# Optimization experiments

Measured on AMD Instinct MI355X. Metric: run time of the kernel, lower is better.

## Reference

```python
import jax, jax.numpy as jnp
import numpy as np

B, S, H = 4, 2048, 1024
HEADS = 16
DFF = 4 * H
EPS = 1e-12


def _layer_norm(x, w, b):
    mu = jnp.mean(x, axis=-1, keepdims=True)
    var = jnp.mean(jnp.square(x - mu), axis=-1, keepdims=True)
    return (x - mu) * jax.lax.rsqrt(var + EPS) * w + b


def setup_inputs() -> dict:
    key = jax.random.key(0)
    ks = jax.random.split(key, 12)
    sc = 0.02
    return {
        "input": jax.random.normal(ks[0], (B, S, H), dtype=jnp.float32),
        "input_mask": jnp.zeros((B, 1, 1, S), dtype=jnp.float32),
        "norm_w": jnp.ones((H,), jnp.float32),
        "norm_b": jnp.zeros((H,), jnp.float32),
        "qkv_w": sc * jax.random.normal(ks[1], (H, 3 * H), jnp.float32),
        "qkv_b": jnp.zeros((3 * H,), jnp.float32),
        "attn_ow": sc * jax.random.normal(ks[2], (H, H), jnp.float32),
        "attn_ob": jnp.zeros((H,), jnp.float32),
        "attn_nw": jnp.ones((H,), jnp.float32),
        "attn_nb": jnp.zeros((H,), jnp.float32),
        "inter_w": sc * jax.random.normal(ks[3], (H, DFF), jnp.float32),
        "inter_b": jnp.zeros((DFF,), jnp.float32),
        "output_w": sc * jax.random.normal(ks[4], (DFF, H), jnp.float32),
        "output_b": jnp.zeros((H,), jnp.float32),
    }


def reference(input, input_mask, norm_w, norm_b, qkv_w, qkv_b, attn_ow, attn_ob,
              attn_nw, attn_nb, inter_w, inter_b, output_w, output_b):
    b, s, h = input.shape
    hd = h // HEADS
    # pre-LN + fused QKV projection (qkv_func)
    x_ln = _layer_norm(input, norm_w, norm_b)
    qkv = x_ln @ qkv_w + qkv_b                      # [b, s, 3h]
    qkv = qkv.reshape(b, s, 3, HEADS, hd)
    q, k, v = qkv[:, :, 0], qkv[:, :, 1], qkv[:, :, 2]   # [b, s, heads, hd]
    # scaled dot-product attention (flash_attn equivalent, non-causal)
    scale = 1.0 / jnp.sqrt(jnp.float32(hd))
    scores = jnp.einsum('bqnd,bknd->bnqk', q, k) * scale  # [b, heads, s, s]
    scores = scores + input_mask                           # additive mask
    probs = jax.nn.softmax(scores, axis=-1)
    ctx = jnp.einsum('bnqk,bknd->bqnd', probs, v).reshape(b, s, h)
    # attention output projection + residual (mlp_func first half)
    attn_out = ctx @ attn_ow + attn_ob + input
    # post-attention LN + FFN (GELU) + residual
    y = _layer_norm(attn_out, attn_nw, attn_nb)
    y = jax.nn.gelu(y @ inter_w + inter_b, approximate=False)
    return y @ output_w + output_b + attn_out
```

## Files before the change

kernel.cpp:

```cpp
#include <hip/hip_runtime.h>
#include <math.h>

typedef __bf16 bf16_t;
typedef bf16_t bf16x8 __attribute__((ext_vector_type(8)));
typedef bf16_t bf16x4 __attribute__((ext_vector_type(4)));
typedef float f32x4 __attribute__((ext_vector_type(4)));
typedef float f32x16 __attribute__((ext_vector_type(16)));

#define BB 4
#define SS 2048
#define HD1 1024
#define NH 16
#define DFF_ 4096

__device__ __forceinline__ void gload_lds16(const bf16_t* g, bf16_t* l) {
  __builtin_amdgcn_global_load_lds(
      (const __attribute__((address_space(1))) void*)g,
      (__attribute__((address_space(3))) void*)l, 16, 0, 0);
}

__device__ __forceinline__ unsigned pack2_bf16(float a, float b) {
  union { bf16_t h[2]; unsigned u; } cv;
  cv.h[0] = (bf16_t)a;
  cv.h[1] = (bf16_t)b;
  return cv.u;
}

__device__ __forceinline__ float block_reduce_sum(float v, float* red) {
  const int lane = threadIdx.x & 63;
  const int wid = threadIdx.x >> 6;
#pragma unroll
  for (int off = 32; off > 0; off >>= 1) v += __shfl_down(v, off, 64);
  if (lane == 0) red[wid] = v;
  __syncthreads();
  float s = red[0] + red[1] + red[2] + red[3];
  __syncthreads();
  return s;
}

__global__ __launch_bounds__(256) void ln_kernel(const float* __restrict__ x,
                                                 const float* __restrict__ w,
                                                 const float* __restrict__ bv,
                                                 bf16_t* __restrict__ out) {
  __shared__ float red[4];
  const size_t row = blockIdx.x;
  const float4 xv = *(const float4*)(x + row * HD1 + threadIdx.x * 4);
  float s = xv.x + xv.y + xv.z + xv.w;
  s = block_reduce_sum(s, red);
  const float mu = s * (1.0f / HD1);
  float4 d;
  d.x = xv.x - mu; d.y = xv.y - mu; d.z = xv.z - mu; d.w = xv.w - mu;
  float sq = d.x * d.x + d.y * d.y + d.z * d.z + d.w * d.w;
  sq = block_reduce_sum(sq, red);
  const float rs = rsqrtf(sq * (1.0f / HD1) + 1e-12f);
  const float4 wv = *(const float4*)(w + threadIdx.x * 4);
  const float4 bb = *(const float4*)(bv + threadIdx.x * 4);
  bf16x4 o;
  o[0] = (bf16_t)(d.x * rs * wv.x + bb.x);
  o[1] = (bf16_t)(d.y * rs * wv.y + bb.y);
  o[2] = (bf16_t)(d.z * rs * wv.z + bb.z);
  o[3] = (bf16_t)(d.w * rs * wv.w + bb.w);
  *(bf16x4*)(out + row * HD1 + threadIdx.x * 4) = o;
}

__global__ __launch_bounds__(256) void wt_kernel(const float* __restrict__ W,
                                                 bf16_t* __restrict__ Wt,
                                                 int K, int N) {
  __shared__ bf16_t T[32][33];
  const int t = threadIdx.x;
  const int n0 = blockIdx.x * 32, k0 = blockIdx.y * 32;
  const int a = t >> 5, c = t & 31;
#pragma unroll
  for (int i = 0; i < 4; ++i) {
    const int kl = a + i * 8;
    T[kl][c] = (bf16_t)W[(size_t)(k0 + kl) * N + n0 + c];
  }
  __syncthreads();
#pragma unroll
  for (int i = 0; i < 4; ++i) {
    const int nl = a + i * 8;
    Wt[(size_t)(n0 + nl) * K + k0 + c] = T[c][nl];
  }
}

__global__ __launch_bounds__(256) void vtrans_kernel(const bf16_t* __restrict__ qkv,
                                                     bf16_t* __restrict__ Vt) {
  const int t = threadIdx.x;
  const int s = blockIdx.x * 256 + t;
  const int head = blockIdx.y, b = blockIdx.z;
  const bf16_t* src = qkv + (size_t)(b * SS + s) * 3072 + 2048 + head * 64;
  bf16_t* dst = Vt + ((size_t)(b * NH + head) * 64) * SS + s;
#pragma unroll
  for (int j = 0; j < 8; ++j) {
    bf16x8 v = *(const bf16x8*)(src + j * 8);
#pragma unroll
    for (int e = 0; e < 8; ++e) dst[(size_t)(j * 8 + e) * SS] = v[e];
  }
}

template <int EPI, bool OBF>
__global__ __launch_bounds__(256) void gemm_bf16(
    const bf16_t* __restrict__ A, const bf16_t* __restrict__ Wt,
    const float* __restrict__ bias, const float* __restrict__ R,
    void* __restrict__ Cout, int M, int N, int K) {
  __shared__ __align__(16) bf16_t As[128 * 32];
  __shared__ __align__(16) bf16_t Bs[128 * 32];
  const int tid = threadIdx.x;
  const int lane = tid & 63;
  const int w = tid >> 6;
  const int wm = (w >> 1) * 64, wn = (w & 1) * 64;
  const int m0 = blockIdx.y * 128, n0 = blockIdx.x * 128;
  const int l15 = lane & 15, l4 = lane >> 4;

  const int arow = tid >> 2;
  const int akof = (tid & 3) * 8;
  const bf16_t* Ap = A + (size_t)(m0 + arow) * K + akof;
  const bf16_t* Bp = Wt + (size_t)(n0 + arow) * K + akof;
  bf16_t* dstA = As + w * 512;
  bf16_t* dstB = Bs + w * 512;

  f32x4 acc[4][4] = {};

  for (int kt = 0; kt < K; kt += 32) {
    __syncthreads();
    gload_lds16(Ap, dstA);
    gload_lds16(Ap + (size_t)64 * K, dstA + 2048);
    gload_lds16(Bp, dstB);
    gload_lds16(Bp + (size_t)64 * K, dstB + 2048);
    __syncthreads();
    bf16x8 af[4], bfr[4];
#pragma unroll
    for (int i = 0; i < 4; ++i)
      af[i] = *(const bf16x8*)(As + (wm + i * 16 + l15) * 32 + l4 * 8);
#pragma unroll
    for (int j = 0; j < 4; ++j)
      bfr[j] = *(const bf16x8*)(Bs + (wn + j * 16 + l15) * 32 + l4 * 8);
#pragma unroll
    for (int i = 0; i < 4; ++i)
#pragma unroll
      for (int j = 0; j < 4; ++j)
        acc[i][j] = __builtin_amdgcn_mfma_f32_16x16x32_bf16(af[i], bfr[j],
                                                            acc[i][j], 0, 0, 0);
    Ap += 32;
    Bp += 32;
  }
#pragma unroll
  for (int j = 0; j < 4; ++j) {
    const int gn = n0 + wn + j * 16 + l15;
    const float bj = bias[gn];
#pragma unroll
    for (int i = 0; i < 4; ++i) {
      const int gm = m0 + wm + i * 16 + l4 * 4;
#pragma unroll
      for (int r = 0; r < 4; ++r) {
        float v = acc[i][j][r] + bj;
        if (EPI == 1) v = 0.5f * v * (1.0f + erff(v * 0.70710678118654752440f));
        if (EPI == 2) v += R[(size_t)(gm + r) * N + gn];
        if (OBF)
          ((bf16_t*)Cout)[(size_t)(gm + r) * N + gn] = (bf16_t)v;
        else
          ((float*)Cout)[(size_t)(gm + r) * N + gn] = v;
      }
    }
  }
}

__global__ __launch_bounds__(256, 2) void attn_kernel(
    const bf16_t* __restrict__ qkv, const bf16_t* __restrict__ Vt,
    const float* __restrict__ mask, bf16_t* __restrict__ ctx) {
  __shared__ __align__(16) bf16_t K_lds[64 * 72];
  __shared__ __align__(16) bf16_t Vt_lds[64 * 72];
  const int tid = threadIdx.x;
  const int lane = tid & 63;
  const int w = tid >> 6;
  const int l31 = lane & 31;
  const int h = lane >> 5;
  const int q0 = blockIdx.x * 128;
  const int head = blockIdx.y;
  const int b = blockIdx.z;
  const int qrow = q0 + w * 32 + l31;

  bf16x8 qf[4];
  {
    const bf16_t* qp = qkv + (size_t)(b * SS + qrow) * 3072 + head * 64 + 8 * h;
#pragma unroll
    for (int ks = 0; ks < 4; ++ks) qf[ks] = *(const bf16x8*)(qp + 16 * ks);
  }

  const int srow = tid >> 2;
  const int scol = (tid & 3) * 16;

  float m = -3.0e38f, l = 0.0f;
  f32x16 cacc0 = {};
  f32x16 cacc1 = {};

  for (int kv0 = 0; kv0 < SS; kv0 += 64) {
    const bf16_t* kp =
        qkv + (size_t)(b * SS + kv0 + srow) * 3072 + 1024 + head * 64 + scol;
    const bf16_t* vp =
        Vt + ((size_t)(b * NH + head) * 64 + srow) * SS + kv0 + scol;
    const bf16x8 k0 = *(const bf16x8*)kp;
    const bf16x8 k1 = *(const bf16x8*)(kp + 8);
    const bf16x8 v0 = *(const bf16x8*)vp;
    const bf16x8 v1 = *(const bf16x8*)(vp + 8);
    float4 mv[8];
#pragma unroll
    for (int k2 = 0; k2 < 8; ++k2)
      mv[k2] = *(const float4*)(mask + (size_t)b * SS + kv0 + 8 * k2 + 4 * h);
    __syncthreads();
    *(bf16x8*)(K_lds + srow * 72 + scol) = k0;
    *(bf16x8*)(K_lds + srow * 72 + scol + 8) = k1;
    *(bf16x8*)(Vt_lds + srow * 72 + scol) = v0;
    *(bf16x8*)(Vt_lds + srow * 72 + scol + 8) = v1;
    __syncthreads();

    f32x16 sacc0 = {};
    f32x16 sacc1 = {};
#pragma unroll
    for (int ks = 0; ks < 4; ++ks) {
      const bf16x8 kf0 = *(const bf16x8*)(K_lds + l31 * 72 + 16 * ks + 8 * h);
      const bf16x8 kf1 =
          *(const bf16x8*)(K_lds + (l31 + 32) * 72 + 16 * ks + 8 * h);
      sacc0 = __builtin_amdgcn_mfma_f32_32x32x16_bf16(kf0, qf[ks], sacc0, 0, 0, 0);
      sacc1 = __builtin_amdgcn_mfma_f32_32x32x16_bf16(kf1, qf[ks], sacc1, 0, 0, 0);
    }

    float ps[32];
    float tmax = -3.0e38f;
#pragma unroll
    for (int r = 0; r < 16; ++r) {
      const float s0 = sacc0[r] * 0.125f + mv[(r >> 2)][r & 3];
      const float s1 = sacc1[r] * 0.125f + mv[(r >> 2) + 4][r & 3];
      ps[r] = s0;
      ps[16 + r] = s1;
      tmax = fmaxf(tmax, fmaxf(s0, s1));
    }
    tmax = fmaxf(tmax, __shfl_xor(tmax, 32, 64));
    if (__any(tmax > m + 8.0f)) {
      const float mnew = fmaxf(m, tmax);
      const float sc = __expf(m - mnew);
      m = mnew;
      l *= sc;
#pragma unroll
      for (int r = 0; r < 16; ++r) {
        const float scr = __shfl(sc, (r & 3) + 8 * (r >> 2) + 4 * h, 64);
        cacc0[r] *= scr;
        cacc1[r] *= scr;
      }
    }
    float ls = 0.0f;
#pragma unroll
    for (int i = 0; i < 32; ++i) {
      ps[i] = __expf(ps[i] - m);
      ls += ps[i];
    }
    l += ls + __shfl_xor(ls, 32, 64);

    unsigned pw0[8], pw1[8];
#pragma unroll
    for (int k = 0; k < 8; ++k) {
      const int base = (k >> 2) * 16 + (k & 3) * 4;
      pw0[k] = pack2_bf16(ps[base + 0], ps[base + 1]);
      pw1[k] = pack2_bf16(ps[base + 2], ps[base + 3]);
    }
#pragma unroll
    for (int t = 0; t < 4; ++t) {
      const unsigned e0 = h ? pw0[2 * t] : pw0[2 * t + 1];
      const unsigned e1 = h ? pw1[2 * t] : pw1[2 * t + 1];
      const unsigned o0 = (unsigned)__shfl_xor((int)e0, 32, 64);
      const unsigned o1 = (unsigned)__shfl_xor((int)e1, 32, 64);
      const unsigned a0 = h ? pw0[2 * t + 1] : pw0[2 * t];
      const unsigned a1 = h ? pw1[2 * t + 1] : pw1[2 * t];
      union { unsigned u[4]; bf16x8 v; } pu;
      pu.u[0] = h ? o0 : a0;
      pu.u[1] = h ? o1 : a1;
      pu.u[2] = h ? a0 : o0;
      pu.u[3] = h ? a1 : o1;
      const bf16x8 vf0 = *(const bf16x8*)(Vt_lds + l31 * 72 + 16 * t + 8 * h);
      const bf16x8 vf1 =
          *(const bf16x8*)(Vt_lds + (l31 + 32) * 72 + 16 * t + 8 * h);
      cacc0 = __builtin_amdgcn_mfma_f32_32x32x16_bf16(pu.v, vf0, cacc0, 0, 0, 0);
      cacc1 = __builtin_amdgcn_mfma_f32_32x32x16_bf16(pu.v, vf1, cacc1, 0, 0, 0);
    }
  }

  const float linv = 1.0f / l;
#pragma unroll
  for (int r = 0; r < 16; ++r) {
    const int rq = (r & 3) + 8 * (r >> 2) + 4 * h;
    const float li = __shfl(linv, rq, 64);
    const int grow = q0 + w * 32 + rq;
    bf16_t* op = ctx + (size_t)(b * SS + grow) * 1024 + head * 64 + l31;
    op[0] = (bf16_t)(cacc0[r] * li);
    op[32] = (bf16_t)(cacc1[r] * li);
  }
}

extern "C" void kernel_launch(void* const* d_in, const int* in_sizes, int n_in,
                              void* d_out, int out_size, void* d_ws, size_t ws_size,
                              hipStream_t stream) {
  const float* input    = (const float*)d_in[0];
  const float* mask     = (const float*)d_in[1];
  const float* norm_w   = (const float*)d_in[2];
  const float* norm_b   = (const float*)d_in[3];
  const float* qkv_w    = (const float*)d_in[4];
  const float* qkv_b    = (const float*)d_in[5];
  const float* attn_ow  = (const float*)d_in[6];
  const float* attn_ob  = (const float*)d_in[7];
  const float* attn_nw  = (const float*)d_in[8];
  const float* attn_nb  = (const float*)d_in[9];
  const float* inter_w  = (const float*)d_in[10];
  const float* inter_b  = (const float*)d_in[11];
  const float* output_w = (const float*)d_in[12];
  const float* output_b = (const float*)d_in[13];

  char* ws = (char*)d_ws;
  const size_t off_xln = 0;
  const size_t off_qkv = 16777216;
  const size_t off_vt  = 67108864;
  const size_t off_ctx = 83886080;
  const size_t off_ao  = 100663296;
  const size_t off_wq  = 134217728;
  const size_t off_wo  = 140509184;
  const size_t off_wi  = 142606336;
  const size_t off_w2  = 150994944;
  const size_t NEED    = 159383552;
  if (ws_size < NEED) return;

  bf16_t* x_ln  = (bf16_t*)(ws + off_xln);
  bf16_t* qkvb  = (bf16_t*)(ws + off_qkv);
  bf16_t* VtB   = (bf16_t*)(ws + off_vt);
  bf16_t* ctxb  = (bf16_t*)(ws + off_ctx);
  bf16_t* y_ln  = (bf16_t*)(ws + off_ctx);
  float*  a_out = (float*)(ws + off_ao);
  bf16_t* wq_t  = (bf16_t*)(ws + off_wq);
  bf16_t* wo_t  = (bf16_t*)(ws + off_wo);
  bf16_t* wi_t  = (bf16_t*)(ws + off_wi);
  bf16_t* w2_t  = (bf16_t*)(ws + off_w2);
  bf16_t* act   = (bf16_t*)(ws + off_xln);

  const int M = BB * SS;

  wt_kernel<<<dim3(3072 / 32, 1024 / 32), 256, 0, stream>>>(qkv_w, wq_t, 1024, 3072);
  wt_kernel<<<dim3(1024 / 32, 1024 / 32), 256, 0, stream>>>(attn_ow, wo_t, 1024, 1024);
  wt_kernel<<<dim3(4096 / 32, 1024 / 32), 256, 0, stream>>>(inter_w, wi_t, 1024, 4096);
  wt_kernel<<<dim3(1024 / 32, 4096 / 32), 256, 0, stream>>>(output_w, w2_t, 4096, 1024);

  ln_kernel<<<M, 256, 0, stream>>>(input, norm_w, norm_b, x_ln);
  gemm_bf16<0, true><<<dim3(3072 / 128, M / 128), 256, 0, stream>>>(
      x_ln, wq_t, qkv_b, nullptr, qkvb, M, 3072, 1024);
  vtrans_kernel<<<dim3(SS / 256, NH, BB), 256, 0, stream>>>(qkvb, VtB);
  attn_kernel<<<dim3(SS / 128, NH, BB), 256, 0, stream>>>(qkvb, VtB, mask, ctxb);
  gemm_bf16<2, false><<<dim3(1024 / 128, M / 128), 256, 0, stream>>>(
      ctxb, wo_t, attn_ob, input, a_out, M, 1024, 1024);
  ln_kernel<<<M, 256, 0, stream>>>(a_out, attn_nw, attn_nb, y_ln);
  gemm_bf16<1, true><<<dim3(4096 / 128, M / 128), 256, 0, stream>>>(
      y_ln, wi_t, inter_b, nullptr, act, M, 4096, 1024);
  gemm_bf16<2, false><<<dim3(1024 / 128, M / 128), 256, 0, stream>>>(
      act, w2_t, output_b, a_out, (float*)d_out, M, 1024, 4096);
}
```

Measured before the change: 531.3 us.

## Double-buffer GEMM LDS tiles with BK=64, swizzle block order, stage bf16 epilogue

```diff
diff --git a/kernel.cpp b/kernel.cpp
--- a/kernel.cpp
+++ b/kernel.cpp
@@ -103,63 +103,118 @@
     const bf16_t* __restrict__ A, const bf16_t* __restrict__ Wt,
     const float* __restrict__ bias, const float* __restrict__ R,
     void* __restrict__ Cout, int M, int N, int K) {
-  __shared__ __align__(16) bf16_t As[128 * 32];
-  __shared__ __align__(16) bf16_t Bs[128 * 32];
+  __shared__ __align__(16) char smem[65536];
+  bf16_t* As = (bf16_t*)smem;
+  bf16_t* Bs = (bf16_t*)(smem + 32768);
   const int tid = threadIdx.x;
   const int lane = tid & 63;
   const int w = tid >> 6;
   const int wm = (w >> 1) * 64, wn = (w & 1) * 64;
-  const int m0 = blockIdx.y * 128, n0 = blockIdx.x * 128;
   const int l15 = lane & 15, l4 = lane >> 4;
 
-  const int arow = tid >> 2;
-  const int akof = (tid & 3) * 8;
-  const bf16_t* Ap = A + (size_t)(m0 + arow) * K + akof;
-  const bf16_t* Bp = Wt + (size_t)(n0 + arow) * K + akof;
-  bf16_t* dstA = As + w * 512;
-  bf16_t* dstB = Bs + w * 512;
-
+  const int gx = gridDim.x;
+  int id = blockIdx.x + gx * blockIdx.y;
+  const int cpx = (gx * gridDim.y) >> 3;
+  id = (id & 7) * cpx + (id >> 3);
+  const int m0 = (id / gx) * 128;
+  const int n0 = (id % gx) * 128;
+
+  const int lrow = tid >> 3;
+  const int lcol = (tid & 7) * 8;
+  const bf16_t* Ag = A + (size_t)(m0 + lrow) * K + lcol;
+  const bf16_t* Bg = Wt + (size_t)(n0 + lrow) * K + lcol;
+  const size_t rstride = (size_t)32 * K;
+
+#pragma unroll
+  for (int c = 0; c < 4; ++c) {
+    gload_lds16(Ag + c * rstride, As + c * 2048 + w * 512);
+    gload_lds16(Bg + c * rstride, Bs + c * 2048 + w * 512);
+  }
+
+  const int NT = K >> 6;
   f32x4 acc[4][4] = {};
 
-  for (int kt = 0; kt < K; kt += 32) {
+  for (int t = 0; t < NT; ++t) {
+    const int cur = t & 1;
     __syncthreads();
-    gload_lds16(Ap, dstA);
-    gload_lds16(Ap + (size_t)64 * K, dstA + 2048);
-    gload_lds16(Bp, dstB);
-    gload_lds16(Bp + (size_t)64 * K, dstB + 2048);
+    if (t + 1 < NT) {
+      const bf16_t* Agn = Ag + (size_t)(t + 1) * 64;
+      const bf16_t* Bgn = Bg + (size_t)(t + 1) * 64;
+      bf16_t* Ad = As + (cur ^ 1) * 8192;
+      bf16_t* Bd = Bs + (cur ^ 1) * 8192;
+#pragma unroll
+      for (int c = 0; c < 4; ++c) {
+        gload_lds16(Agn + c * rstride, Ad + c * 2048 + w * 512);
+        gload_lds16(Bgn + c * rstride, Bd + c * 2048 + w * 512);
+      }
+    }
+    const bf16_t* Ab = As + cur * 8192;
+    const bf16_t* Bb = Bs + cur * 8192;
+    bf16x8 af[2][4], bfr[2][4];
+#pragma unroll
+    for (int ks = 0; ks < 2; ++ks) {
+#pragma unroll
+      for (int i = 0; i < 4; ++i)
+        af[ks][i] =
+            *(const bf16x8*)(Ab + (wm + i * 16 + l15) * 64 + ks * 32 + l4 * 8);
+#pragma unroll
+      for (int j = 0; j < 4; ++j)
+        bfr[ks][j] =
+            *(const bf16x8*)(Bb + (wn + j * 16 + l15) * 64 + ks * 32 + l4 * 8);
+    }
+#pragma unroll
+    for (int ks = 0; ks < 2; ++ks)
+#pragma unroll
+      for (int i = 0; i < 4; ++i)
+#pragma unroll
+        for (int j = 0; j < 4; ++j)
+          acc[i][j] = __builtin_amdgcn_mfma_f32_16x16x32_bf16(
+              af[ks][i], bfr[ks][j], acc[i][j], 0, 0, 0);
+  }
+
+  if (OBF) {
     __syncthreads();
-    bf16x8 af[4], bfr[4];
-#pragma unroll
-    for (int i = 0; i < 4; ++i)
-      af[i] = *(const bf16x8*)(As + (wm + i * 16 + l15) * 32 + l4 * 8);
-#pragma unroll
-    for (int j = 0; j < 4; ++j)
-      bfr[j] = *(const bf16x8*)(Bs + (wn + j * 16 + l15) * 32 + l4 * 8);
-#pragma unroll
-    for (int i = 0; i < 4; ++i)
-#pragma unroll
-      for (int j = 0; j < 4; ++j)
-        acc[i][j] = __builtin_amdgcn_mfma_f32_16x16x32_bf16(af[i], bfr[j],
-                                                            acc[i][j], 0, 0, 0);
-    Ap += 32;
-    Bp += 32;
-  }
-#pragma unroll
-  for (int j = 0; j < 4; ++j) {
-    const int gn = n0 + wn + j * 16 + l15;
-    const float bj = bias[gn];
-#pragma unroll
-    for (int i = 0; i < 4; ++i) {
-      const int gm = m0 + wm + i * 16 + l4 * 4;
-#pragma unroll
-      for (int r = 0; r < 4; ++r) {
-        float v = acc[i][j][r] + bj;
-        if (EPI == 1) v = 0.5f * v * (1.0f + erff(v * 0.70710678118654752440f));
-        if (EPI == 2) v += R[(size_t)(gm + r) * N + gn];
-        if (OBF)
-          ((bf16_t*)Cout)[(size_t)(gm + r) * N + gn] = (bf16_t)v;
-        else
-          ((float*)Cout)[(size_t)(gm + r) * N + gn] = v;
+    float* Cs = (float*)smem;
+#pragma unroll
+    for (int j = 0; j < 4; ++j) {
+      const float bj = bias[n0 + wn + j * 16 + l15];
+#pragma unroll
+      for (int i = 0; i < 4; ++i)
+#pragma unroll
+        for (int r = 0; r < 4; ++r) {
+          float v = acc[i][j][r] + bj;
+          if (EPI == 1)
+            v = 0.5f * v * (1.0f + erff(v * 0.70710678118654752440f));
+          Cs[(wm + i * 16 + l4 * 4 + r) * 128 + wn + j * 16 + l15] = v;
+        }
+    }
+    __syncthreads();
+    bf16_t* Cb = (bf16_t*)Cout;
+#pragma unroll
+    for (int p = 0; p < 16; ++p) {
+      const int idx = p * 256 + tid;
+      const int row = idx >> 5, c4 = idx & 31;
+      const f32x4 v = *(const f32x4*)(Cs + row * 128 + c4 * 4);
+      bf16x4 o;
+      o[0] = (bf16_t)v[0]; o[1] = (bf16_t)v[1];
+      o[2] = (bf16_t)v[2]; o[3] = (bf16_t)v[3];
+      *(bf16x4*)(Cb + (size_t)(m0 + row) * N + n0 + c4 * 4) = o;
+    }
+  } else {
+    float* Cf = (float*)Cout;
+#pragma unroll
+    for (int j = 0; j < 4; ++j) {
+      const int gn = n0 + wn + j * 16 + l15;
+      const float bj = bias[gn];
+#pragma unroll
+      for (int i = 0; i < 4; ++i) {
+        const int gm = m0 + wm + i * 16 + l4 * 4;
+#pragma unroll
+        for (int r = 0; r < 4; ++r) {
+          float v = acc[i][j][r] + bj;
+          if (EPI == 2) v += R[(size_t)(gm + r) * N + gn];
+          Cf[(size_t)(gm + r) * N + gn] = v;
+        }
       }
     }
   }
```

Result: faster. 499.1 us (-6.1%).
